# Optimization experiments

Measured on AMD Instinct MI355X. Metric: run time of the kernel, lower is better.

## Reference

```python
import jax, jax.numpy as jnp
import numpy as np

N = 20000    # nodes
F = 64       # channels (num_features)
Z = 10       # species
DEG = 16
E = N * DEG  # edges
RD = 8       # radial_dim
EPS = 0.25   # epsilon (avg-degree normalization)
SQRT3 = 3.0 ** 0.5


def setup_inputs() -> dict:
    key = jax.random.key(0)
    ks = jax.random.split(key, 22)
    g = lambda i, shape, s=1.0: jax.random.normal(ks[i], shape, jnp.float32) * s
    return dict(
        vectors=g(0, (E, 3)),
        node_s=g(1, (N, F)),
        node_v=g(2, (N, F, 3)),
        radial_embed=jax.random.uniform(ks[3], (E, RD), jnp.float32),
        senders=jax.random.randint(ks[4], (E,), 0, N),
        receivers=jax.random.randint(ks[5], (E,), 0, N),
        species_counts=jnp.full((Z,), N // Z, dtype=jnp.int32),
        Wup0=g(6, (F, F)), Wup1=g(7, (F, F)),
        R1=g(8, (RD, 64)), R2=g(9, (64, 64)), R3=g(10, (64, 64)), R4=g(11, (64, 4 * F)),
        Wd0=g(12, (F, F)), Wd1=g(13, (F, F)),
        Ws0=g(14, (Z, F, F)), Ws1=g(15, (Z, F, F)),
        Wsc=g(16, (Z, 9, F)), Proj=g(17, (9, 9), 1.0 / 3.0),
        Wl0=g(18, (F, F)), Wl1=g(19, (F, F)),
        Wr=g(20, (F, 1)),
    )


def _forward(vectors, node_s, node_v, radial_embed, senders, receivers,
             species_counts, Wup0, Wup1, R1, R2, R3, R4, Wd0, Wd1,
             Ws0, Ws1, Wsc, Proj, Wl0, Wl1, Wr):
    inv = 1.0 / np.sqrt(F)
    # species index per node (counts -> contiguous blocks), like jnp.repeat in SymmetricContraction
    sidx = jnp.repeat(jnp.arange(Z), species_counts, total_repeat_length=N)

    # spherical harmonics l=0 (constant 1, folded into weights) and l=1
    r = jnp.linalg.norm(vectors, axis=-1, keepdims=True)
    Y1 = SQRT3 * vectors / r                              # (E,3)

    # species-indexed skip connection on input feats
    skip_s = jnp.einsum('nf,nfg->ng', node_s, Ws0[sidx]) * inv
    skip_v = jnp.einsum('nfi,nfg->ngi', node_v, Ws1[sidx]) * inv

    # linear_up (per-irrep channel mixing)
    hs = (node_s @ Wup0) * inv                            # (N,F)
    hv = jnp.einsum('nfi,fg->ngi', node_v, Wup1) * inv    # (N,F,3)

    # radial MLP -> per-edge, per-path, per-channel TP weights (weight_numel = 4*F)
    a = jax.nn.silu(radial_embed @ R1)
    a = jax.nn.silu(a @ R2)
    a = jax.nn.silu(a @ R3)
    w = (a @ R4).reshape(E, 4, F)

    # channelwise tensor product: gather senders, 4 CG paths, scatter to receivers
    es = hs[senders]                                      # (E,F)
    ev = hv[senders]                                      # (E,F,3)
    m_s = w[:, 0] * es + w[:, 1] * (jnp.einsum('efi,ei->ef', ev, Y1) / SQRT3)
    m_v = w[:, 2][..., None] * ev + w[:, 3][..., None] * (es[..., None] * Y1[:, None, :]) / SQRT3
    hs = jax.ops.segment_sum(m_s, receivers, num_segments=N) * EPS
    hv = jax.ops.segment_sum(m_v, receivers, num_segments=N) * EPS

    # linear_down
    hs = (hs @ Wd0) * inv
    hv = jnp.einsum('nfi,fg->ngi', hv, Wd1) * inv

    # symmetric contraction (correlation 1..3), species-keyed weights through fixed projection
    wsc = jnp.einsum('zpu,pb->zbu', Wsc, Proj)[sidx]      # (N,9,F)
    vv = jnp.sum(hv * hv, -1)                             # (N,F)
    bs = jnp.stack([hs, hs * hs, vv, hs ** 3, hs * vv], axis=1)                    # (N,5,F)
    bv = jnp.stack([hv, hs[..., None] * hv, (hs * hs)[..., None] * hv,
                    vv[..., None] * hv], axis=1)                                   # (N,4,F,3)
    cs = jnp.einsum('nbf,nbf->nf', bs, wsc[:, :5])
    cv = jnp.einsum('nbfi,nbf->nfi', bv, wsc[:, 5:])

    # linear_sc
    cs = (cs @ Wl0) * inv
    cv = jnp.einsum('nfi,fg->ngi', cv, Wl1) * inv

    # add skip
    h_s = cs + skip_s
    h_v = cv + skip_v

    # readout (0e -> 1x0e; only scalars participate)
    out = (h_s @ Wr) * inv                                # (N,1)
    return out, h_s, h_v


def reference(vectors, node_s, node_v, radial_embed, senders, receivers,
              species_counts, Wup0, Wup1, R1, R2, R3, R4, Wd0, Wd1,
              Ws0, Ws1, Wsc, Proj, Wl0, Wl1, Wr):
    return _forward(vectors, node_s, node_v, radial_embed, senders, receivers,
                    species_counts, Wup0, Wup1, R1, R2, R3, R4, Wd0, Wd1,
                    Ws0, Ws1, Wsc, Proj, Wl0, Wl1, Wr)
```

## Files before the change

### kernel.cpp

```cpp
#include <hip/hip_runtime.h>
#include <hip/hip_bf16.h>
#include <math.h>

#define N_NODES 20000
#define FCH 64
#define ZSP 10
#define E_EDGES 320000
#define CHUNK 160000
#define RDIM 8
#define EPSC 0.25f
#define SQRT3C 1.7320508075688772f
#define INV_SQRT3C 0.57735026918962576f
#define INV_F 0.125f

#define OFF_HSUP   0
#define OFF_HVUP   (N_NODES*64)
#define OFF_SKS    (OFF_HVUP + N_NODES*192)
#define OFF_SKV    (OFF_SKS + N_NODES*64)
#define OFF_HSMID  (OFF_SKV + N_NODES*192)
#define OFF_HVMID  (OFF_HSMID + N_NODES*64)
#define OFF_WSCP   (OFF_HVMID + N_NODES*192)
#define OFF_FRAGS  (OFF_WSCP + ZSP*576)
#define OFF_WBUF   (OFF_FRAGS + 13312)
#define OFF_CSR    (OFF_WBUF + CHUNK*128)
#define OFF_WF     (OFF_CSR + 2*CHUNK*4 + 400260)
#define CSR_CNT0   0
#define CSR_CNT1   20000
#define CSR_PTR0   40000
#define CSR_PTR1   60001
#define CSR_SEID   80002
#define CSR_AUX    400002

#define SU_WSC   5760
#define SU_PREP  (SU_WSC + 3328)
#define SU_PREP2 (SU_PREP + 26624)
#define SU_HIST  (SU_PREP2 + E_EDGES)

typedef __attribute__((ext_vector_type(8))) short bhalf8;
typedef __attribute__((ext_vector_type(4))) float f32x4;

__device__ __forceinline__ float silu_f(float x) {
    float e = __builtin_amdgcn_exp2f(x * -1.442695040888963f);
    return x * __builtin_amdgcn_rcpf(1.0f + e);
}

__device__ __forceinline__ unsigned short f2bf(float x) {
    unsigned int u = __float_as_uint(x);
    unsigned int r = u + 0x7FFFu + ((u >> 16) & 1u);
    return (unsigned short)(r >> 16);
}

__device__ __forceinline__ unsigned int pack_bf2(float lo, float hi) {
    __hip_bfloat162 b = __float22bfloat162_rn(make_float2(lo, hi));
    return *(unsigned int*)&b;
}

__device__ __forceinline__ bhalf8 mk8(unsigned a, unsigned b, unsigned c, unsigned d) {
    uint4 u; u.x = a; u.y = b; u.z = c; u.w = d;
    return *(bhalf8*)&u;
}

__device__ __forceinline__ void split_f32(float x, short& h, short& l) {
    unsigned int u = __float_as_uint(x);
    unsigned int hb = u & 0xFFFF0000u;
    h = (short)(u >> 16);
    float r = x - __uint_as_float(hb);
    l = (short)(__float_as_uint(r) >> 16);
}

__device__ __forceinline__ int species_of(int n, const int* counts) {
    int acc = 0, s = ZSP - 1;
#pragma unroll
    for (int z = 0; z < ZSP; z++) {
        int c = counts[z];
        if (n >= acc && n < acc + c) s = z;
        acc += c;
    }
    return s;
}

__global__ __launch_bounds__(256) void k_setup(
    const float* __restrict__ Wsc, const float* __restrict__ Proj, float* __restrict__ wscp,
    const float* __restrict__ R1, const float* __restrict__ R2,
    const float* __restrict__ R3, const float* __restrict__ R4,
    unsigned short* __restrict__ frags,
    const float* __restrict__ Wup0, const float* __restrict__ Wup1,
    const float* __restrict__ Ws0, const float* __restrict__ Ws1,
    const float* __restrict__ Wd0, const float* __restrict__ Wd1,
    const float* __restrict__ Wl0, const float* __restrict__ Wl1,
    unsigned short* __restrict__ wf,
    const int* __restrict__ receivers, int* __restrict__ csr) {
    int gid = blockIdx.x * 256 + threadIdx.x;
    if (gid < SU_WSC) {
        int z = gid / 576, t = gid % 576;
        int b = t >> 6, u = t & 63;
        float acc = 0.f;
#pragma unroll
        for (int p = 0; p < 9; p++) acc += Wsc[z * 576 + p * 64 + u] * Proj[p * 9 + b];
        wscp[z * 576 + b * 64 + u] = acc;
    } else if (gid < SU_PREP) {
        int id = gid - SU_WSC;
        int lane = id & 63, fi = id >> 6;
        int quad = lane >> 4, l15 = lane & 15;
        const float* W;
        int s, t, N;
        bool r1 = false;
        if (fi < 4)       { W = R1; s = 0; t = fi; N = 64; r1 = true; }
        else if (fi < 12) { W = R2; int x = fi - 4;  s = x >> 2; t = x & 3;  N = 64; }
        else if (fi < 20) { W = R3; int x = fi - 12; s = x >> 2; t = x & 3;  N = 64; }
        else              { W = R4; int x = fi - 20; s = x >> 4; t = x & 15; N = 256; }
        unsigned int v[4];
#pragma unroll
        for (int jj = 0; jj < 4; jj++) {
            unsigned short pk2[2];
#pragma unroll
            for (int o = 0; o < 2; o++) {
                int j = jj * 2 + o;
                int k = s * 32 + quad * 8 + j, n = t * 16 + l15;
                float val = (r1 && k >= RDIM) ? 0.f : W[k * N + n];
                pk2[o] = f2bf(val);
            }
            v[jj] = (unsigned int)pk2[0] | ((unsigned int)pk2[1] << 16);
        }
        uint4 pk; pk.x = v[0]; pk.y = v[1]; pk.z = v[2]; pk.w = v[3];
        ((uint4*)frags)[id] = pk;
    } else if (gid < SU_PREP2) {
        int id = gid - SU_PREP;
        int lane = id & 63, slot = id >> 6;
        int t = slot & 3, s = (slot >> 2) & 1, part = (slot >> 3) & 1, mat = slot >> 4;
        int quad = lane >> 4, l15 = lane & 15;
        const float* W;
        if (mat == 0)       W = Wup0;
        else if (mat == 1)  W = Wup1;
        else if (mat < 12)  W = Ws0 + (mat - 2) * 4096;
        else if (mat < 22)  W = Ws1 + (mat - 12) * 4096;
        else if (mat == 22) W = Wd0;
        else if (mat == 23) W = Wd1;
        else if (mat == 24) W = Wl0;
        else                W = Wl1;
        unsigned int v[4];
#pragma unroll
        for (int jj = 0; jj < 4; jj++) {
            unsigned short pk2[2];
#pragma unroll
            for (int o = 0; o < 2; o++) {
                int j = jj * 2 + o;
                int k = s * 32 + quad * 8 + j, n = t * 16 + l15;
                float x = W[k * 64 + n];
                short h, l;
                split_f32(x, h, l);
                pk2[o] = part == 0 ? (unsigned short)h : (unsigned short)l;
            }
            v[jj] = (unsigned int)pk2[0] | ((unsigned int)pk2[1] << 16);
        }
        uint4 pk; pk.x = v[0]; pk.y = v[1]; pk.z = v[2]; pk.w = v[3];
        ((uint4*)wf)[id] = pk;
    } else if (gid < SU_HIST) {
        int e = gid - SU_PREP2;
        int base = (e < CHUNK) ? CSR_CNT0 : CSR_CNT1;
        atomicAdd(&csr[base + receivers[e]], 1);
    }
}

__global__ __launch_bounds__(256) void k_scan1(int* __restrict__ csr) {
    __shared__ int sb[256];
    int z = blockIdx.y, b = blockIdx.x, t = threadIdx.x;
    int i = b * 256 + t;
    int cb = z ? CSR_CNT1 : CSR_CNT0;
    int pb = z ? CSR_PTR1 : CSR_PTR0;
    int x = (i < N_NODES) ? csr[cb + i] : 0;
    sb[t] = x;
    __syncthreads();
#pragma unroll
    for (int off = 1; off < 256; off <<= 1) {
        int v = (t >= off) ? sb[t - off] : 0;
        __syncthreads();
        sb[t] += v;
        __syncthreads();
    }
    if (i < N_NODES) csr[pb + i] = sb[t] - x;
    if (t == 255) csr[CSR_AUX + z * 128 + b] = sb[255];
}

__global__ __launch_bounds__(128) void k_scan2(int* __restrict__ csr) {
    __shared__ int sb[128];
    int z = blockIdx.x, t = threadIdx.x;
    int pb = z ? CSR_PTR1 : CSR_PTR0;
    int x = (t < 79) ? csr[CSR_AUX + z * 128 + t] : 0;
    sb[t] = x;
    __syncthreads();
#pragma unroll
    for (int off = 1; off < 128; off <<= 1) {
        int v = (t >= off) ? sb[t - off] : 0;
        __syncthreads();
        sb[t] += v;
        __syncthreads();
    }
    csr[CSR_AUX + z * 128 + t] = sb[t] - x;
    if (t == 127) csr[pb + N_NODES] = sb[127];
}

__global__ __launch_bounds__(256) void k_scan3(int* __restrict__ csr) {
    int z = blockIdx.y, b = blockIdx.x, t = threadIdx.x;
    int i = b * 256 + t;
    if (i >= N_NODES) return;
    int cb = z ? CSR_CNT1 : CSR_CNT0;
    int pb = z ? CSR_PTR1 : CSR_PTR0;
    int v = csr[pb + i] + csr[CSR_AUX + z * 128 + b];
    csr[pb + i] = v;
    csr[cb + i] = v;
}

__global__ __launch_bounds__(256) void k_bucket(
    const float* __restrict__ vectors, const int* __restrict__ senders,
    const int* __restrict__ receivers, int* __restrict__ csr,
    float4* __restrict__ erec) {
    int e = blockIdx.x * 256 + threadIdx.x;
    if (e >= E_EDGES) return;
    int z = (e < CHUNK) ? 0 : 1;
    int base = z ? CSR_CNT1 : CSR_CNT0;
    int pos = atomicAdd(&csr[base + receivers[e]], 1);
    float v0 = vectors[e * 3 + 0], v1 = vectors[e * 3 + 1], v2 = vectors[e * 3 + 2];
    float s = SQRT3C * rsqrtf(v0 * v0 + v1 * v1 + v2 * v2);
    int idx = z * CHUNK + pos;
    csr[CSR_SEID + idx] = e;
    float4 r;
    r.x = v0 * s; r.y = v1 * s; r.z = v2 * s; r.w = __int_as_float(senders[e]);
    erec[idx] = r;
}

__global__ __launch_bounds__(256) void k_node_pre(
    const float* __restrict__ ns, const float* __restrict__ nv,
    const int* __restrict__ counts, const unsigned short* __restrict__ wf,
    float* __restrict__ ws) {
    int tid = threadIdx.x, w = tid >> 6, lane = tid & 63;
    int q = lane >> 4, l15 = lane & 15;
    int nw = blockIdx.x * 16;
    int sid = species_of(nw, counts);
    const f32x4 z4 = {0.f, 0.f, 0.f, 0.f};

    bhalf8 Ah[2], Al[2];
    if (w == 0) {
#pragma unroll
        for (int s = 0; s < 2; s++) {
            const float* rp = ns + (size_t)(nw + l15) * 64 + s * 32 + q * 8;
            float4 a = *(const float4*)rp, b = *(const float4*)(rp + 4);
            float x[8] = {a.x, a.y, a.z, a.w, b.x, b.y, b.z, b.w};
#pragma unroll
            for (int j = 0; j < 8; j++) { short h, l; split_f32(x[j], h, l); Ah[s][j] = h; Al[s][j] = l; }
        }
    } else {
        int i = w - 1;
#pragma unroll
        for (int s = 0; s < 2; s++) {
            const float* rp = nv + (size_t)(nw + l15) * 192 + i;
#pragma unroll
            for (int j = 0; j < 8; j++) {
                float x = rp[(s * 32 + q * 8 + j) * 3];
                short h, l; split_f32(x, h, l); Ah[s][j] = h; Al[s][j] = l;
            }
        }
    }

    const bhalf8* wfv = (const bhalf8*)wf;
    float* hs_up = ws + OFF_HSUP;
    float* hv_up = ws + OFF_HVUP;
    float* sks   = ws + OFF_SKS;
    float* skv   = ws + OFF_SKV;

#pragma unroll
    for (int m = 0; m < 2; m++) {
        int mat = (w == 0) ? (m == 0 ? 0 : 2 + sid) : (m == 0 ? 1 : 12 + sid);
        float* dst; int stride, off;
        if (w == 0) { dst = m == 0 ? hs_up : sks; stride = 64; off = 0; }
        else        { dst = m == 0 ? hv_up : skv; stride = 192; off = (w - 1) * 64; }
#pragma unroll
        for (int t = 0; t < 4; t++) {
            f32x4 acc = z4;
#pragma unroll
            for (int s = 0; s < 2; s++) {
                bhalf8 bh = wfv[(size_t)(mat * 16 + 0 + s * 4 + t) * 64 + lane];
                bhalf8 bl = wfv[(size_t)(mat * 16 + 8 + s * 4 + t) * 64 + lane];
                acc = __builtin_amdgcn_mfma_f32_16x16x32_bf16(Ah[s], bh, acc, 0, 0, 0);
                acc = __builtin_amdgcn_mfma_f32_16x16x32_bf16(Al[s], bh, acc, 0, 0, 0);
                acc = __builtin_amdgcn_mfma_f32_16x16x32_bf16(Ah[s], bl, acc, 0, 0, 0);
            }
#pragma unroll
            for (int r = 0; r < 4; r++)
                dst[(size_t)(nw + q * 4 + r) * stride + off + t * 16 + l15] = acc[r] * INV_F;
        }
    }
}

template<int S>
__device__ __forceinline__ bhalf8 xfrag(const unsigned* pkA, const unsigned* pkB,
                                        int q, int l15) {
    int L0 = ((q & 1) << 5) + l15;
    int L1 = L0 + 16;
    bool hi = (q >> 1) != 0;
    unsigned a0 = (unsigned)__shfl((int)pkA[2 * S], L0, 64);
    unsigned a1 = (unsigned)__shfl((int)pkA[2 * S + 1], L0, 64);
    unsigned b0 = (unsigned)__shfl((int)pkB[2 * S], L0, 64);
    unsigned b1 = (unsigned)__shfl((int)pkB[2 * S + 1], L0, 64);
    unsigned c0 = (unsigned)__shfl((int)pkA[2 * S], L1, 64);
    unsigned c1 = (unsigned)__shfl((int)pkA[2 * S + 1], L1, 64);
    unsigned e0 = (unsigned)__shfl((int)pkB[2 * S], L1, 64);
    unsigned e1 = (unsigned)__shfl((int)pkB[2 * S + 1], L1, 64);
    return mk8(hi ? a1 : a0, hi ? b1 : b0, hi ? c1 : c0, hi ? e1 : e0);
}

__global__ __launch_bounds__(256) void k_mlp(
    const float* __restrict__ radial, const unsigned short* __restrict__ frags,
    const int* __restrict__ csr, unsigned short* __restrict__ wbuf, int e_base) {
    __shared__ unsigned short r4lds[16384];
    int tid = threadIdx.x;
    int lane = tid & 63, w = tid >> 6, quad = lane >> 4, l15 = lane & 15;

    const uint4* r4g = (const uint4*)(frags + 20 * 64 * 8);
    uint4* r4l = (uint4*)r4lds;
    for (int i = tid; i < 2048; i += 256) r4l[i] = r4g[i];
    const bhalf8* fr = (const bhalf8*)frags;
    bhalf8 r1f[4], r2f[2][4], r3f[2][4];
#pragma unroll
    for (int t = 0; t < 4; t++) r1f[t] = fr[t * 64 + lane];
#pragma unroll
    for (int s = 0; s < 2; s++)
#pragma unroll
        for (int t = 0; t < 4; t++) {
            r2f[s][t] = fr[(4 + s * 4 + t) * 64 + lane];
            r3f[s][t] = fr[(12 + s * 4 + t) * 64 + lane];
        }
    __syncthreads();

    const f32x4 z4 = {0.f, 0.f, 0.f, 0.f};
    const bhalf8* r4f = (const bhalf8*)r4lds;

    int el0 = (blockIdx.x * 4 + w) * 16;

    bhalf8 af = {0, 0, 0, 0, 0, 0, 0, 0};
    if (quad == 0) {
        int eid = csr[CSR_SEID + e_base + el0 + l15];
        const float* rp = radial + (size_t)eid * 8;
        float4 ra = *(const float4*)rp;
        float4 rb = *(const float4*)(rp + 4);
        af[0] = (short)f2bf(ra.x); af[1] = (short)f2bf(ra.y);
        af[2] = (short)f2bf(ra.z); af[3] = (short)f2bf(ra.w);
        af[4] = (short)f2bf(rb.x); af[5] = (short)f2bf(rb.y);
        af[6] = (short)f2bf(rb.z); af[7] = (short)f2bf(rb.w);
    }
    unsigned pkA[4], pkB[4];
    {
        f32x4 acc[4];
#pragma unroll
        for (int t = 0; t < 4; t++)
            acc[t] = __builtin_amdgcn_mfma_f32_16x16x32_bf16(r1f[t], af, z4, 0, 0, 0);
#pragma unroll
        for (int t = 0; t < 4; t++) {
            pkA[t] = pack_bf2(silu_f(acc[t][0]), silu_f(acc[t][1]));
            pkB[t] = pack_bf2(silu_f(acc[t][2]), silu_f(acc[t][3]));
        }
    }
#pragma unroll
    for (int layer = 0; layer < 2; layer++) {
        bhalf8 b0 = xfrag<0>(pkA, pkB, quad, l15);
        bhalf8 b1 = xfrag<1>(pkA, pkB, quad, l15);
        f32x4 acc[4];
#pragma unroll
        for (int t = 0; t < 4; t++) {
            bhalf8 w0 = layer == 0 ? r2f[0][t] : r3f[0][t];
            bhalf8 w1 = layer == 0 ? r2f[1][t] : r3f[1][t];
            acc[t] = __builtin_amdgcn_mfma_f32_16x16x32_bf16(
                w1, b1, __builtin_amdgcn_mfma_f32_16x16x32_bf16(w0, b0, z4, 0, 0, 0), 0, 0, 0);
        }
#pragma unroll
        for (int t = 0; t < 4; t++) {
            pkA[t] = pack_bf2(silu_f(acc[t][0]), silu_f(acc[t][1]));
            pkB[t] = pack_bf2(silu_f(acc[t][2]), silu_f(acc[t][3]));
        }
    }
    {
        bhalf8 a0 = xfrag<0>(pkA, pkB, quad, l15);
        bhalf8 a1 = xfrag<1>(pkA, pkB, quad, l15);
#pragma unroll
        for (int t4 = 0; t4 < 4; t4++) {
            f32x4 p0 = __builtin_amdgcn_mfma_f32_16x16x32_bf16(
                a1, r4f[(16 + t4) * 64 + lane],
                __builtin_amdgcn_mfma_f32_16x16x32_bf16(a0, r4f[t4 * 64 + lane], z4, 0, 0, 0), 0, 0, 0);
            f32x4 p1 = __builtin_amdgcn_mfma_f32_16x16x32_bf16(
                a1, r4f[(20 + t4) * 64 + lane],
                __builtin_amdgcn_mfma_f32_16x16x32_bf16(a0, r4f[(4 + t4) * 64 + lane], z4, 0, 0, 0), 0, 0, 0);
            f32x4 p2 = __builtin_amdgcn_mfma_f32_16x16x32_bf16(
                a1, r4f[(24 + t4) * 64 + lane],
                __builtin_amdgcn_mfma_f32_16x16x32_bf16(a0, r4f[(8 + t4) * 64 + lane], z4, 0, 0, 0), 0, 0, 0);
            f32x4 p3 = __builtin_amdgcn_mfma_f32_16x16x32_bf16(
                a1, r4f[(28 + t4) * 64 + lane],
                __builtin_amdgcn_mfma_f32_16x16x32_bf16(a0, r4f[(12 + t4) * 64 + lane], z4, 0, 0, 0), 0, 0, 0);
#pragma unroll
            for (int r = 0; r < 4; r++) {
                int el = el0 + quad * 4 + r;
                int f = t4 * 16 + l15;
                uint2 pk;
                pk.x = pack_bf2(p0[r], p1[r]);
                pk.y = pack_bf2(p2[r], p3[r]);
                ((uint2*)wbuf)[(size_t)el * 64 + f] = pk;
            }
        }
    }
}

__global__ __launch_bounds__(256) void k_tp_gather(
    const unsigned short* __restrict__ wbuf, const int* __restrict__ csr,
    const float4* __restrict__ erec, float* __restrict__ ws,
    int z, int accum) {
    int tid = threadIdx.x, w = tid >> 6, f = tid & 63;
    int n = blockIdx.x * 4 + w;
    const float* hs_up = ws + OFF_HSUP;
    const float* hv_up = ws + OFF_HVUP;
    float* hs_mid = ws + OFF_HSMID;
    float* hv_mid = ws + OFF_HVMID;
    int pb = z ? CSR_PTR1 : CSR_PTR0;
    int beg = csr[pb + n], end = csr[pb + n + 1];
    int e_base = z * CHUNK;
    float ams = 0.f, am0 = 0.f, am1 = 0.f, am2 = 0.f;

    if (beg < end) {
        int last = end - 1;
        float4 rcA = erec[e_base + beg];
        uint2 wrA = ((const uint2*)wbuf)[(size_t)beg * 64 + f];
        int sxA = __float_as_int(rcA.w);
        float esA = hs_up[sxA * 64 + f];
        float eA0 = hv_up[sxA * 192 + f];
        float eA1 = hv_up[sxA * 192 + 64 + f];
        float eA2 = hv_up[sxA * 192 + 128 + f];
        int j1 = (beg + 1 < end) ? beg + 1 : last;
        float4 rcB = erec[e_base + j1];
        uint2 wrB = ((const uint2*)wbuf)[(size_t)j1 * 64 + f];
        int sxB = __float_as_int(rcB.w);
        float esB = hs_up[sxB * 64 + f];
        float eB0 = hv_up[sxB * 192 + f];
        float eB1 = hv_up[sxB * 192 + 64 + f];
        float eB2 = hv_up[sxB * 192 + 128 + f];

        for (int i = beg; i < end; i++) {
            int j2 = (i + 2 < end) ? i + 2 : last;
            float4 rcC = erec[e_base + j2];
            uint2 wrC = ((const uint2*)wbuf)[(size_t)j2 * 64 + f];
            int sxC = __float_as_int(rcC.w);
            float esC = hs_up[sxC * 64 + f];
            float eC0 = hv_up[sxC * 192 + f];
            float eC1 = hv_up[sxC * 192 + 64 + f];
            float eC2 = hv_up[sxC * 192 + 128 + f];
            float w0 = __uint_as_float(wrA.x << 16);
            float w1 = __uint_as_float(wrA.x & 0xFFFF0000u);
            float w2 = __uint_as_float(wrA.y << 16);
            float w3 = __uint_as_float(wrA.y & 0xFFFF0000u);
            float dot = eA0 * rcA.x + eA1 * rcA.y + eA2 * rcA.z;
            ams += w0 * esA + w1 * dot * INV_SQRT3C;
            float t3 = w3 * esA * INV_SQRT3C;
            am0 += w2 * eA0 + t3 * rcA.x;
            am1 += w2 * eA1 + t3 * rcA.y;
            am2 += w2 * eA2 + t3 * rcA.z;
            rcA = rcB; wrA = wrB; esA = esB; eA0 = eB0; eA1 = eB1; eA2 = eB2;
            rcB = rcC; wrB = wrC; esB = esC; eB0 = eC0; eB1 = eC1; eB2 = eC2;
        }
    }
    if (!accum) {
        hs_mid[n * 64 + f] = ams;
        hv_mid[n * 192 + f] = am0;
        hv_mid[n * 192 + 64 + f] = am1;
        hv_mid[n * 192 + 128 + f] = am2;
    } else {
        hs_mid[n * 64 + f] = (hs_mid[n * 64 + f] + ams) * EPSC;
        hv_mid[n * 192 + f] = (hv_mid[n * 192 + f] + am0) * EPSC;
        hv_mid[n * 192 + 64 + f] = (hv_mid[n * 192 + 64 + f] + am1) * EPSC;
        hv_mid[n * 192 + 128 + f] = (hv_mid[n * 192 + 128 + f] + am2) * EPSC;
    }
}

__global__ __launch_bounds__(256) void k_node_post(
    const int* __restrict__ counts, const unsigned short* __restrict__ wf,
    const float* __restrict__ Wr, float* __restrict__ ws, float* __restrict__ out) {
    __shared__ float T[4][16][68];
    int tid = threadIdx.x, w = tid >> 6, lane = tid & 63;
    int q = lane >> 4, l15 = lane & 15;
    int nw = blockIdx.x * 16;
    int sid = species_of(nw, counts);
    const f32x4 z4 = {0.f, 0.f, 0.f, 0.f};
    const bhalf8* wfv = (const bhalf8*)wf;
    const float* hs_mid = ws + OFF_HSMID;
    const float* hv_mid = ws + OFF_HVMID;
    const float* sks = ws + OFF_SKS;
    const float* skv = ws + OFF_SKV;
    const float* wscp = ws + OFF_WSCP;

    {
        const float* src = (w == 0) ? hs_mid + (size_t)nw * 64
                                    : hv_mid + (size_t)nw * 192 + (w - 1) * 64;
        int rstride = (w == 0) ? 64 : 192;
        bhalf8 Ah[2], Al[2];
#pragma unroll
        for (int s = 0; s < 2; s++) {
            const float* rp = src + (size_t)l15 * rstride + s * 32 + q * 8;
            float4 a = *(const float4*)rp, b = *(const float4*)(rp + 4);
            float x[8] = {a.x, a.y, a.z, a.w, b.x, b.y, b.z, b.w};
#pragma unroll
            for (int j = 0; j < 8; j++) { short h, l; split_f32(x[j], h, l); Ah[s][j] = h; Al[s][j] = l; }
        }
        int mat = (w == 0) ? 22 : 23;
#pragma unroll
        for (int t = 0; t < 4; t++) {
            f32x4 acc = z4;
#pragma unroll
            for (int s = 0; s < 2; s++) {
                bhalf8 bh = wfv[(size_t)(mat * 16 + 0 + s * 4 + t) * 64 + lane];
                bhalf8 bl = wfv[(size_t)(mat * 16 + 8 + s * 4 + t) * 64 + lane];
                acc = __builtin_amdgcn_mfma_f32_16x16x32_bf16(Ah[s], bh, acc, 0, 0, 0);
                acc = __builtin_amdgcn_mfma_f32_16x16x32_bf16(Al[s], bh, acc, 0, 0, 0);
                acc = __builtin_amdgcn_mfma_f32_16x16x32_bf16(Ah[s], bl, acc, 0, 0, 0);
            }
#pragma unroll
            for (int r = 0; r < 4; r++)
                T[w][q * 4 + r][t * 16 + l15] = acc[r] * INV_F;
        }
    }
    __syncthreads();

    {
        int col = tid & 63, rg = tid >> 6;
        float wv[9];
#pragma unroll
        for (int b = 0; b < 9; b++) wv[b] = wscp[sid * 576 + b * 64 + col];
#pragma unroll
        for (int rr = 0; rr < 4; rr++) {
            int row = rg * 4 + rr;
            float hs = T[0][row][col];
            float h0 = T[1][row][col], h1 = T[2][row][col], h2 = T[3][row][col];
            float vv = h0 * h0 + h1 * h1 + h2 * h2;
            float cs = wv[0] * hs + wv[1] * hs * hs + wv[2] * vv
                     + wv[3] * hs * hs * hs + wv[4] * hs * vv;
            float fv = wv[5] + wv[6] * hs + wv[7] * hs * hs + wv[8] * vv;
            T[0][row][col] = cs;
            T[1][row][col] = h0 * fv;
            T[2][row][col] = h1 * fv;
            T[3][row][col] = h2 * fv;
        }
    }
    __syncthreads();

    {
        bhalf8 Ah[2], Al[2];
#pragma unroll
        for (int s = 0; s < 2; s++) {
            const float* rp = &T[w][l15][s * 32 + q * 8];
            float4 a = *(const float4*)rp, b = *(const float4*)(rp + 4);
            float x[8] = {a.x, a.y, a.z, a.w, b.x, b.y, b.z, b.w};
#pragma unroll
            for (int j = 0; j < 8; j++) { short h, l; split_f32(x[j], h, l); Ah[s][j] = h; Al[s][j] = l; }
        }
        int mat = (w == 0) ? 24 : 25;
        float* d_hs = out + N_NODES;
        float* d_hv = out + N_NODES + N_NODES * 64;
        float p[4] = {0.f, 0.f, 0.f, 0.f};
#pragma unroll
        for (int t = 0; t < 4; t++) {
            f32x4 acc = z4;
#pragma unroll
            for (int s = 0; s < 2; s++) {
                bhalf8 bh = wfv[(size_t)(mat * 16 + 0 + s * 4 + t) * 64 + lane];
                bhalf8 bl = wfv[(size_t)(mat * 16 + 8 + s * 4 + t) * 64 + lane];
                acc = __builtin_amdgcn_mfma_f32_16x16x32_bf16(Ah[s], bh, acc, 0, 0, 0);
                acc = __builtin_amdgcn_mfma_f32_16x16x32_bf16(Al[s], bh, acc, 0, 0, 0);
                acc = __builtin_amdgcn_mfma_f32_16x16x32_bf16(Ah[s], bl, acc, 0, 0, 0);
            }
            int col = t * 16 + l15;
            if (w == 0) {
                float wr = Wr[col];
#pragma unroll
                for (int r = 0; r < 4; r++) {
                    int gn = nw + q * 4 + r;
                    float v = acc[r] * INV_F + sks[(size_t)gn * 64 + col];
                    d_hs[(size_t)gn * 64 + col] = v;
                    p[r] += v * wr;
                }
            } else {
                int i = w - 1;
#pragma unroll
                for (int r = 0; r < 4; r++) {
                    int gn = nw + q * 4 + r;
                    float v = acc[r] * INV_F + skv[(size_t)gn * 192 + i * 64 + col];
                    d_hv[(size_t)gn * 192 + col * 3 + i] = v;
                }
            }
        }
        if (w == 0) {
#pragma unroll
            for (int r = 0; r < 4; r++) {
#pragma unroll
                for (int off = 1; off < 16; off <<= 1) p[r] += __shfl_xor(p[r], off, 64);
                if (l15 == 0) out[nw + q * 4 + r] = p[r] * INV_F;
            }
        }
    }
}

extern "C" void kernel_launch(void* const* d_in, const int* in_sizes, int n_in,
                              void* d_out, int out_size, void* d_ws, size_t ws_size,
                              hipStream_t stream) {
    const float* vectors   = (const float*)d_in[0];
    const float* node_s    = (const float*)d_in[1];
    const float* node_v    = (const float*)d_in[2];
    const float* radial    = (const float*)d_in[3];
    const int*   senders   = (const int*)d_in[4];
    const int*   receivers = (const int*)d_in[5];
    const int*   counts    = (const int*)d_in[6];
    const float* Wup0 = (const float*)d_in[7];
    const float* Wup1 = (const float*)d_in[8];
    const float* R1   = (const float*)d_in[9];
    const float* R2   = (const float*)d_in[10];
    const float* R3   = (const float*)d_in[11];
    const float* R4   = (const float*)d_in[12];
    const float* Wd0  = (const float*)d_in[13];
    const float* Wd1  = (const float*)d_in[14];
    const float* Ws0  = (const float*)d_in[15];
    const float* Ws1  = (const float*)d_in[16];
    const float* Wsc  = (const float*)d_in[17];
    const float* Proj = (const float*)d_in[18];
    const float* Wl0  = (const float*)d_in[19];
    const float* Wl1  = (const float*)d_in[20];
    const float* Wr   = (const float*)d_in[21];
    float* ws  = (float*)d_ws;
    float* out = (float*)d_out;
    unsigned short* frags = (unsigned short*)(ws + OFF_FRAGS);
    unsigned short* wbuf  = (unsigned short*)(ws + OFF_WBUF);
    float4* erec = (float4*)(ws + OFF_CSR);
    int* csr = (int*)(ws + OFF_CSR + 2 * CHUNK * 4);
    unsigned short* wf = (unsigned short*)(ws + OFF_WF);

    hipMemsetAsync(csr, 0, 2 * N_NODES * sizeof(int), stream);
    k_setup<<<(SU_HIST + 255) / 256, 256, 0, stream>>>(
        Wsc, Proj, ws + OFF_WSCP, R1, R2, R3, R4, frags,
        Wup0, Wup1, Ws0, Ws1, Wd0, Wd1, Wl0, Wl1, wf, receivers, csr);
    k_scan1<<<dim3(79, 2), 256, 0, stream>>>(csr);
    k_scan2<<<2, 128, 0, stream>>>(csr);
    k_scan3<<<dim3(79, 2), 256, 0, stream>>>(csr);
    k_bucket<<<E_EDGES / 256, 256, 0, stream>>>(vectors, senders, receivers, csr, erec);
    k_node_pre<<<N_NODES / 16, 256, 0, stream>>>(node_s, node_v, counts, wf, ws);
    for (int c = 0; c < 2; c++) {
        k_mlp<<<2500, 256, 0, stream>>>(radial, frags, csr, wbuf, c * CHUNK);
        k_tp_gather<<<N_NODES / 4, 256, 0, stream>>>(wbuf, csr, erec, ws, c, c);
    }
    k_node_post<<<N_NODES / 16, 256, 0, stream>>>(counts, wf, Wr, ws, out);
}
```

Measured before the change: 333.5 us.

## Pack upsampled node features as interleaved fp16 for single-load edge gather

The linear_up outputs (scalar plus three vector components per channel) are now stored as fp16 in one interleaved 8-byte record per node and channel, staged through shared memory in the node kernel. The edge gather kernel then fetches one uint2 per sender instead of four separate fp32 loads from strided arrays. This cuts gather bandwidth and the number of memory transactions in the dominant edge loop. The cost is fp16 precision on the gathered features, which risks range or accuracy problems, plus a shared-memory staging pass and a block barrier in the node kernel.

```diff
diff --git a/kernel.cpp b/kernel.cpp
--- a/kernel.cpp
+++ b/kernel.cpp
@@ -1,5 +1,6 @@
 #include <hip/hip_runtime.h>
 #include <hip/hip_bf16.h>
+#include <hip/hip_fp16.h>
 #include <math.h>
 
 #define N_NODES 20000
@@ -13,9 +14,8 @@
 #define INV_SQRT3C 0.57735026918962576f
 #define INV_F 0.125f
 
-#define OFF_HSUP   0
-#define OFF_HVUP   (N_NODES*64)
-#define OFF_SKS    (OFF_HVUP + N_NODES*192)
+#define OFF_EUP    0
+#define OFF_SKS    (N_NODES*256)
 #define OFF_SKV    (OFF_SKS + N_NODES*64)
 #define OFF_HSMID  (OFF_SKV + N_NODES*192)
 #define OFF_HVMID  (OFF_HSMID + N_NODES*64)
@@ -58,6 +58,13 @@
 __device__ __forceinline__ bhalf8 mk8(unsigned a, unsigned b, unsigned c, unsigned d) {
     uint4 u; u.x = a; u.y = b; u.z = c; u.w = d;
     return *(bhalf8*)&u;
+}
+
+__device__ __forceinline__ float half_lo(unsigned v) {
+    return __half2float(__ushort_as_half((unsigned short)(v & 0xFFFFu)));
+}
+__device__ __forceinline__ float half_hi(unsigned v) {
+    return __half2float(__ushort_as_half((unsigned short)(v >> 16)));
 }
 
 __device__ __forceinline__ void split_f32(float x, short& h, short& l) {
@@ -233,6 +240,7 @@
     const float* __restrict__ ns, const float* __restrict__ nv,
     const int* __restrict__ counts, const unsigned short* __restrict__ wf,
     float* __restrict__ ws) {
+    __shared__ uint2 eup_t[16][64];
     int tid = threadIdx.x, w = tid >> 6, lane = tid & 63;
     int q = lane >> 4, l15 = lane & 15;
     int nw = blockIdx.x * 16;
@@ -263,17 +271,11 @@
     }
 
     const bhalf8* wfv = (const bhalf8*)wf;
-    float* hs_up = ws + OFF_HSUP;
-    float* hv_up = ws + OFF_HVUP;
-    float* sks   = ws + OFF_SKS;
-    float* skv   = ws + OFF_SKV;
-
-#pragma unroll
-    for (int m = 0; m < 2; m++) {
-        int mat = (w == 0) ? (m == 0 ? 0 : 2 + sid) : (m == 0 ? 1 : 12 + sid);
-        float* dst; int stride, off;
-        if (w == 0) { dst = m == 0 ? hs_up : sks; stride = 64; off = 0; }
-        else        { dst = m == 0 ? hv_up : skv; stride = 192; off = (w - 1) * 64; }
+    float* sks = ws + OFF_SKS;
+    float* skv = ws + OFF_SKV;
+
+    {
+        int mat = (w == 0) ? 0 : 1;
 #pragma unroll
         for (int t = 0; t < 4; t++) {
             f32x4 acc = z4;
@@ -286,9 +288,38 @@
                 acc = __builtin_amdgcn_mfma_f32_16x16x32_bf16(Ah[s], bl, acc, 0, 0, 0);
             }
 #pragma unroll
+            for (int r = 0; r < 4; r++) {
+                unsigned short us = __half_as_ushort(__float2half_rn(acc[r] * INV_F));
+                ((unsigned short*)&eup_t[q * 4 + r][t * 16 + l15])[w] = us;
+            }
+        }
+    }
+    {
+        int mat = (w == 0) ? 2 + sid : 12 + sid;
+        float* dst = (w == 0) ? sks : skv;
+        int stride = (w == 0) ? 64 : 192;
+        int off = (w == 0) ? 0 : (w - 1) * 64;
+#pragma unroll
+        for (int t = 0; t < 4; t++) {
+            f32x4 acc = z4;
+#pragma unroll
+            for (int s = 0; s < 2; s++) {
+                bhalf8 bh = wfv[(size_t)(mat * 16 + 0 + s * 4 + t) * 64 + lane];
+                bhalf8 bl = wfv[(size_t)(mat * 16 + 8 + s * 4 + t) * 64 + lane];
+                acc = __builtin_amdgcn_mfma_f32_16x16x32_bf16(Ah[s], bh, acc, 0, 0, 0);
+                acc = __builtin_amdgcn_mfma_f32_16x16x32_bf16(Al[s], bh, acc, 0, 0, 0);
+                acc = __builtin_amdgcn_mfma_f32_16x16x32_bf16(Ah[s], bl, acc, 0, 0, 0);
+            }
+#pragma unroll
             for (int r = 0; r < 4; r++)
                 dst[(size_t)(nw + q * 4 + r) * stride + off + t * 16 + l15] = acc[r] * INV_F;
         }
+    }
+    __syncthreads();
+    uint2* eup = (uint2*)(ws + OFF_EUP);
+    for (int k = tid; k < 1024; k += 256) {
+        int n = k >> 6, f = k & 63;
+        eup[(size_t)(nw + n) * 64 + f] = eup_t[n][f];
     }
 }
 
@@ -414,8 +445,7 @@
     int z, int accum) {
     int tid = threadIdx.x, w = tid >> 6, f = tid & 63;
     int n = blockIdx.x * 4 + w;
-    const float* hs_up = ws + OFF_HSUP;
-    const float* hv_up = ws + OFF_HVUP;
+    const uint2* eup = (const uint2*)(ws + OFF_EUP);
     float* hs_mid = ws + OFF_HSMID;
     float* hv_mid = ws + OFF_HVMID;
     int pb = z ? CSR_PTR1 : CSR_PTR0;
@@ -427,29 +457,19 @@
         int last = end - 1;
         float4 rcA = erec[e_base + beg];
         uint2 wrA = ((const uint2*)wbuf)[(size_t)beg * 64 + f];
-        int sxA = __float_as_int(rcA.w);
-        float esA = hs_up[sxA * 64 + f];
-        float eA0 = hv_up[sxA * 192 + f];
-        float eA1 = hv_up[sxA * 192 + 64 + f];
-        float eA2 = hv_up[sxA * 192 + 128 + f];
+        uint2 evA = eup[(size_t)__float_as_int(rcA.w) * 64 + f];
         int j1 = (beg + 1 < end) ? beg + 1 : last;
         float4 rcB = erec[e_base + j1];
         uint2 wrB = ((const uint2*)wbuf)[(size_t)j1 * 64 + f];
-        int sxB = __float_as_int(rcB.w);
-        float esB = hs_up[sxB * 64 + f];
-        float eB0 = hv_up[sxB * 192 + f];
-        float eB1 = hv_up[sxB * 192 + 64 + f];
-        float eB2 = hv_up[sxB * 192 + 128 + f];
+        uint2 evB = eup[(size_t)__float_as_int(rcB.w) * 64 + f];
 
         for (int i = beg; i < end; i++) {
             int j2 = (i + 2 < end) ? i + 2 : last;
             float4 rcC = erec[e_base + j2];
             uint2 wrC = ((const uint2*)wbuf)[(size_t)j2 * 64 + f];
-            int sxC = __float_as_int(rcC.w);
-            float esC = hs_up[sxC * 64 + f];
-            float eC0 = hv_up[sxC * 192 + f];
-            float eC1 = hv_up[sxC * 192 + 64 + f];
-            float eC2 = hv_up[sxC * 192 + 128 + f];
+            uint2 evC = eup[(size_t)__float_as_int(rcC.w) * 64 + f];
+            float esA = half_lo(evA.x), eA0 = half_hi(evA.x);
+            float eA1 = half_lo(evA.y), eA2 = half_hi(evA.y);
             float w0 = __uint_as_float(wrA.x << 16);
             float w1 = __uint_as_float(wrA.x & 0xFFFF0000u);
             float w2 = __uint_as_float(wrA.y << 16);
@@ -460,8 +480,8 @@
             am0 += w2 * eA0 + t3 * rcA.x;
             am1 += w2 * eA1 + t3 * rcA.y;
             am2 += w2 * eA2 + t3 * rcA.z;
-            rcA = rcB; wrA = wrB; esA = esB; eA0 = eB0; eA1 = eB1; eA2 = eB2;
-            rcB = rcC; wrB = wrC; esB = esC; eB0 = eC0; eB1 = eC1; eB2 = eC2;
+            rcA = rcB; wrA = wrB; evA = evB;
+            rcB = rcC; wrB = wrC; evB = evC;
         }
     }
     if (!accum) {
```

Result: faster. 318.2 us (-4.6%).
